# Kernel optimization log

Hardware: AMD Instinct MI355X
Metric: run time of the kernel (lower is better)

## Reference

```python
import jax, jax.numpy as jnp
import numpy as np

LOG2PI = float(np.log(2.0 * np.pi))
NUM_GROUPS = 32
WEIGHTS_THRESHOLD = 0.01
ACTIVATION_THRESHOLD = 1e-9


def _cdist(a, b):
    # a: (..., N, 3), b: (..., M, 3) -> (..., N, M) euclidean distances
    d2 = (jnp.sum(a * a, -1)[..., :, None]
          + jnp.sum(b * b, -1)[..., None, :]
          - 2.0 * jnp.einsum('...nd,...md->...nm', a, b))
    return jnp.sqrt(jnp.maximum(d2, 0.0))


def setup_inputs() -> dict:
    key = jax.random.key(0)
    ks = jax.random.split(key, 7)
    B, V, O, G = 16, 778, 8192, NUM_GROUPS
    verts = jax.random.normal(ks[0], (B, V, 3), jnp.float32)
    anchor_verts = jax.random.normal(ks[1], (B, G, 3), jnp.float32)
    obj_pts = jax.random.normal(ks[2], (B, O, 3), jnp.float32)
    raw = jax.random.normal(ks[3], (B, G, 12), jnp.float32)
    mean = raw[..., :3]
    M = raw[..., 3:].reshape(B, G, 3, 3)
    cov = jnp.einsum('bgij,bgkj->bgik', M, M) + 1e-2 * jnp.eye(3, dtype=jnp.float32)
    contact_gaussians = jnp.concatenate([mean, cov.reshape(B, G, 9)], axis=-1)
    obj_normals = jax.random.normal(ks[4], (B, O, 6), jnp.float32)
    init_verts = jax.random.normal(ks[5], (V, 3), jnp.float32)
    init_anchors = jax.random.normal(ks[6], (G, 3), jnp.float32)
    return dict(verts=verts, anchor_verts=anchor_verts, obj_pts=obj_pts,
                contact_gaussians=contact_gaussians, obj_normals=obj_normals,
                init_verts=init_verts, init_anchors=init_anchors, K=5)


def reference(verts, anchor_verts, obj_pts, contact_gaussians, obj_normals,
              init_verts, init_anchors, K):
    B, V, _ = verts.shape
    G = NUM_GROUPS
    # __init__: assign each vertex to its closest anchor (partition into 32 groups)
    gid = jnp.argmin(_cdist(init_verts, init_anchors), axis=-1)  # (V,)

    # KNN: K smallest distances vertex -> object points
    neigh = _cdist(verts, obj_pts)                 # (B, V, O)
    knn = -jax.lax.top_k(-neigh, K)[0]             # (B, V, K)

    # Per-group MVN log-prob for every vertex (G=32 small, V=778 small)
    mean = contact_gaussians[:, :, :3] + anchor_verts          # (B, G, 3)
    cov = contact_gaussians[:, :, 3:].reshape(B, G, 3, 3)
    L = jnp.linalg.cholesky(cov)                               # (B, G, 3, 3)
    diff = verts[:, None, :, :] - mean[:, :, None, :]          # (B, G, V, 3)
    y = jax.scipy.linalg.solve_triangular(L[:, :, None], diff[..., None], lower=True)[..., 0]
    maha = jnp.sum(y * y, -1)                                  # (B, G, V)
    half_logdet = jnp.sum(jnp.log(jnp.diagonal(L, axis1=-2, axis2=-1)), -1)  # (B, G)
    logp = -0.5 * (maha + 3.0 * LOG2PI) - half_logdet[:, :, None]
    w_all = jnp.exp(logp)                                      # (B, G, V)
    # pick each vertex's own group's weight
    idx = jnp.broadcast_to(gid[None, None, :], (B, 1, V))
    w = jnp.take_along_axis(w_all, idx, axis=1)[:, 0]          # (B, V)

    # per-group min/max normalization (masked, groups partition the vertices)
    grp_mask = gid[None, :] == jnp.arange(G)[:, None]          # (G, V)
    seg_min = jnp.min(jnp.where(grp_mask[None], w[:, None, :], jnp.inf), -1)   # (B, G)
    seg_max = jnp.max(jnp.where(grp_mask[None], w[:, None, :], -jnp.inf), -1)  # (B, G)
    mn = seg_min[:, gid]
    mx = seg_max[:, gid]
    wn = (w - mn) / (mx - mn)
    wn = jnp.where(wn > WEIGHTS_THRESHOLD, wn, 0.0)

    # group activation: torch.allclose(cg[:, i], 0) over whole batch -> zero weight
    active = jnp.any(jnp.abs(contact_gaussians) > ACTIVATION_THRESHOLD, axis=(0, 2))  # (G,)
    eff = jnp.where(active[gid][None, :], wn, 0.0)             # (B, V)
    distances = knn * eff[..., None]
    d_mean = jnp.mean(distances)

    # penetration regularizer using nearest object normal
    ovd = _cdist(verts, obj_normals[..., :3])                  # (B, V, O)
    nn_idx = jnp.argmin(ovd, -1)                               # (B, V)
    nn = jnp.take_along_axis(obj_normals, nn_idx[..., None], axis=1)  # (B, V, 6)
    roots = nn[..., :3] - 0.002 * nn[..., 3:]
    dp = jnp.einsum('bvi,bvi->bv', nn[..., 3:], verts - roots)
    pen = jnp.mean(jax.nn.relu(-dp))
    return (d_mean, pen)
```

## Files before the change

### kernel.cpp

```cpp
#include <hip/hip_runtime.h>
#include <math.h>

#define BB 16
#define VV 778
#define OO 8192
#define GG 32
#define KNN 5
#define THREE_LOG2PI 5.513631199228036f

#define MED3 __builtin_amdgcn_fmed3f

__device__ __forceinline__ void insert5_med3(float (&t)[KNN], float s) {
    t[4] = MED3(s, t[3], t[4]);
    t[3] = MED3(s, t[2], t[3]);
    t[2] = MED3(s, t[1], t[2]);
    t[1] = MED3(s, t[0], t[1]);
    t[0] = fminf(t[0], s);
}

__device__ __forceinline__ void merge5_med3(float (&m)[KNN], const float (&b)[KNN]) {
    m[4] = MED3(b[0], m[3], m[4]);
    m[3] = MED3(b[0], m[2], m[3]);
    m[2] = MED3(b[0], m[1], m[2]);
    m[1] = MED3(b[0], m[0], m[1]);
    m[0] = fminf(m[0], b[0]);
    m[4] = MED3(b[1], m[3], m[4]);
    m[3] = MED3(b[1], m[2], m[3]);
    m[2] = MED3(b[1], m[1], m[2]);
    m[1] = fminf(m[1], b[1]);
    m[4] = MED3(b[2], m[3], m[4]);
    m[3] = MED3(b[2], m[2], m[3]);
    m[2] = fminf(m[2], b[2]);
    m[4] = MED3(b[3], m[3], m[4]);
    m[3] = fminf(m[3], b[3]);
    m[4] = fminf(m[4], b[4]);
}

__device__ __forceinline__ unsigned int fkey(float s) {
    unsigned int u = __float_as_uint(s);
    unsigned int m = (u & 0x80000000u) ? 0xFFFFFFFFu : 0x80000000u;
    return u ^ m;
}

template <int LOGP1, int LOGP2>
__global__ __launch_bounds__(256) void scan_kernel(
    const float* __restrict__ verts,
    const float* __restrict__ anchor_verts,
    const float* __restrict__ obj_pts,
    const float* __restrict__ contact_gaussians,
    const float* __restrict__ obj_normals,
    const float* __restrict__ init_verts,
    const float* __restrict__ init_anchors,
    int* __restrict__ gid_ws,
    float* __restrict__ active_ws,
    float* __restrict__ segmn,
    float* __restrict__ segmx,
    float* __restrict__ w_ws,
    float* __restrict__ top5,
    unsigned long long* __restrict__ amin,
    float* __restrict__ out) {
    constexpr int P1 = 1 << LOGP1;
    constexpr int NPTS1 = OO >> LOGP1;
    constexpr int CH1 = (NPTS1 < 512) ? NPTS1 : 512;
    constexpr int P2 = 1 << LOGP2;
    constexpr int NPTS2 = OO >> LOGP2;
    constexpr int CH2 = (NPTS2 < 512) ? NPTS2 : 512;
    constexpr int CHMAX = (CH1 > CH2) ? CH1 : CH2;

    __shared__ float4 tile[CHMAX];
    __shared__ float anc[GG * 4];
    __shared__ float cholb[GG * 10];
    __shared__ unsigned short gidl[VV];
    __shared__ unsigned int smn[GG], smx[GG];

    int tid = threadIdx.x;
    int bid = blockIdx.x;

    if (bid < BB * P1) {
        int p = bid & (P1 - 1);
        int b = bid >> LOGP1;

        float X[4], Y[4], Z[4];
#pragma unroll
        for (int s = 0; s < 4; ++s) {
            int v = tid + s * 256;
            if (v >= VV) v = VV - 1;
            const float* vp = verts + ((size_t)b * VV + v) * 3;
            X[s] = -2.0f * vp[0];
            Y[s] = -2.0f * vp[1];
            Z[s] = -2.0f * vp[2];
        }

        float t[4][KNN];
#pragma unroll
        for (int s = 0; s < 4; ++s)
#pragma unroll
            for (int k = 0; k < KNN; ++k) t[s][k] = INFINITY;

        const float* pb = obj_pts + ((size_t)b * OO + p * NPTS1) * 3;
        for (int c0 = 0; c0 < NPTS1; c0 += CH1) {
            for (int j = tid; j < CH1; j += 256) {
                const float* q = pb + (size_t)(c0 + j) * 3;
                float a0 = q[0], a1 = q[1], a2 = q[2];
                tile[j] = make_float4(a0, a1, a2, a0 * a0 + a1 * a1 + a2 * a2);
            }
            __syncthreads();
#pragma unroll 4
            for (int i = 0; i < CH1; ++i) {
                float4 q = tile[i];
#pragma unroll
                for (int s = 0; s < 4; ++s) {
                    float sv = fmaf(X[s], q.x, fmaf(Y[s], q.y, fmaf(Z[s], q.z, q.w)));
                    insert5_med3(t[s], sv);
                }
            }
            __syncthreads();
        }
        {
            size_t base = ((size_t)(b * P1 + p) * KNN) * VV;
#pragma unroll
            for (int s = 0; s < 4; ++s) {
                int v = tid + s * 256;
                if (v < VV) {
#pragma unroll
                    for (int k = 0; k < KNN; ++k)
                        top5[base + (size_t)k * VV + v] = t[s][k];
                }
            }
        }
        return;
    }

    {
        int sub = bid - BB * P1;
        int p = sub & (P2 - 1);
        int b = sub >> LOGP2;

        bool wduty = (p == 0);
        bool aduty = (p == 1 && b == 0);
        if (wduty || aduty) {
            if (tid < GG) {
                float x = init_anchors[tid * 3 + 0];
                float y = init_anchors[tid * 3 + 1];
                float z = init_anchors[tid * 3 + 2];
                anc[tid * 4 + 0] = x; anc[tid * 4 + 1] = y;
                anc[tid * 4 + 2] = z; anc[tid * 4 + 3] = x * x + y * y + z * z;
                smn[tid] = 0x7F800000u;
                smx[tid] = 0u;
                if (wduty) {
                    const float* cg2 = contact_gaussians + ((size_t)b * GG + tid) * 12;
                    const float* av = anchor_verts + ((size_t)b * GG + tid) * 3;
                    float c00 = cg2[3];
                    float c10 = cg2[6], c11 = cg2[7];
                    float c20 = cg2[9], c21 = cg2[10], c22 = cg2[11];
                    float L00 = sqrtf(c00);
                    float L10 = c10 / L00;
                    float L20 = c20 / L00;
                    float L11 = sqrtf(c11 - L10 * L10);
                    float L21 = (c21 - L20 * L10) / L11;
                    float L22 = sqrtf(c22 - L20 * L20 - L21 * L21);
                    float* c = cholb + tid * 10;
                    c[0] = L00; c[1] = L10; c[2] = L11;
                    c[3] = L20; c[4] = L21; c[5] = L22;
                    c[6] = logf(L00) + logf(L11) + logf(L22);
                    c[7] = cg2[0] + av[0];
                    c[8] = cg2[1] + av[1];
                    c[9] = cg2[2] + av[2];
                }
            }
            __syncthreads();
            for (int v = tid; v < VV; v += 256) {
                float x = init_verts[v * 3 + 0];
                float y = init_verts[v * 3 + 1];
                float z = init_verts[v * 3 + 2];
                float vv = x * x + y * y + z * z;
                float best = INFINITY;
                int bg = 0;
                for (int g = 0; g < GG; ++g) {
                    float d2 = vv + anc[g * 4 + 3] -
                               2.0f * (x * anc[g * 4 + 0] + y * anc[g * 4 + 1] + z * anc[g * 4 + 2]);
                    d2 = fmaxf(d2, 0.0f);
                    if (d2 < best) { best = d2; bg = g; }
                }
                gidl[v] = (unsigned short)bg;
                if (aduty) gid_ws[v] = bg;
            }
            __syncthreads();
            if (wduty) {
                for (int v = tid; v < VV; v += 256) {
                    int g = gidl[v];
                    const float* c = cholb + g * 10;
                    const float* vp = verts + ((size_t)b * VV + v) * 3;
                    float d0 = vp[0] - c[7];
                    float d1 = vp[1] - c[8];
                    float d2 = vp[2] - c[9];
                    float y0 = d0 / c[0];
                    float y1 = (d1 - c[1] * y0) / c[2];
                    float y2 = (d2 - c[3] * y0 - c[4] * y1) / c[5];
                    float maha = y0 * y0 + y1 * y1 + y2 * y2;
                    float wv = expf(-0.5f * (maha + THREE_LOG2PI) - c[6]);
                    w_ws[(size_t)b * VV + v] = wv;
                    unsigned int u = __float_as_uint(wv);
                    atomicMin(&smn[g], u);
                    atomicMax(&smx[g], u);
                }
                __syncthreads();
                if (tid < GG) {
                    segmn[b * GG + tid] = __uint_as_float(smn[tid]);
                    segmx[b * GG + tid] = __uint_as_float(smx[tid]);
                }
            }
            if (aduty) {
                if (tid < GG) {
                    int any = 0;
                    for (int bb = 0; bb < BB && !any; ++bb) {
                        for (int c = 0; c < 12; ++c) {
                            if (fabsf(contact_gaussians[((size_t)bb * GG + tid) * 12 + c]) > 1e-9f) {
                                any = 1;
                                break;
                            }
                        }
                    }
                    active_ws[tid] = any ? 1.0f : 0.0f;
                }
                if (tid == 0) { out[0] = 0.0f; out[1] = 0.0f; }
            }
            __syncthreads();
        }

        float X[4], Y[4], Z[4];
#pragma unroll
        for (int s = 0; s < 4; ++s) {
            int v = tid + s * 256;
            if (v >= VV) v = VV - 1;
            const float* vp = verts + ((size_t)b * VV + v) * 3;
            X[s] = -2.0f * vp[0];
            Y[s] = -2.0f * vp[1];
            Z[s] = -2.0f * vp[2];
        }

        float bs[4];
        int bi[4];
#pragma unroll
        for (int s = 0; s < 4; ++s) { bs[s] = INFINITY; bi[s] = 0; }

        const float* nbp = obj_normals + ((size_t)b * OO + p * NPTS2) * 6;
        for (int c0 = 0; c0 < NPTS2; c0 += CH2) {
            for (int j = tid; j < CH2; j += 256) {
                const float* r = nbp + (size_t)(c0 + j) * 6;
                float b0 = r[0], b1 = r[1], b2 = r[2];
                tile[j] = make_float4(b0, b1, b2, b0 * b0 + b1 * b1 + b2 * b2);
            }
            __syncthreads();
#pragma unroll 4
            for (int i = 0; i < CH2; ++i) {
                float4 n = tile[i];
                int gi = c0 + i;
#pragma unroll
                for (int s = 0; s < 4; ++s) {
                    float u = fmaf(X[s], n.x, fmaf(Y[s], n.y, fmaf(Z[s], n.z, n.w)));
                    if (u < bs[s]) { bs[s] = u; bi[s] = gi; }
                }
            }
            __syncthreads();
        }
#pragma unroll
        for (int s = 0; s < 4; ++s) {
            int v = tid + s * 256;
            if (v < VV) {
                unsigned long long key =
                    ((unsigned long long)fkey(bs[s]) << 32) |
                    (unsigned int)(p * NPTS2 + bi[s]);
                atomicMin(&amin[(size_t)b * VV + v], key);
            }
        }
    }
}

template <int LOGP1>
__global__ __launch_bounds__(256) void finalize_kernel(
    const float* __restrict__ top5,
    const unsigned long long* __restrict__ amin,
    const float* __restrict__ obj_normals,
    const float* __restrict__ verts,
    const int* __restrict__ gid,
    const float* __restrict__ w,
    const float* __restrict__ segmn,
    const float* __restrict__ segmx,
    const float* __restrict__ active,
    float* __restrict__ out) {
    constexpr int P1 = 1 << LOGP1;
    constexpr int NM1 = (P1 + 3) / 4;
    constexpr int NCH = (VV + 63) / 64;

    __shared__ float mt[4][KNN][64];
    __shared__ float rd[256], rp[256];

    int tid = threadIdx.x;
    int pi = tid >> 6;
    int vi = tid & 63;
    int b = blockIdx.x / NCH;
    int chunk = blockIdx.x - b * NCH;
    int v = chunk * 64 + vi;
    bool valid = v < VV;

    float m[KNN];
#pragma unroll
    for (int k = 0; k < KNN; ++k) m[k] = INFINITY;
    if (valid) {
#pragma unroll
        for (int r = 0; r < NM1; ++r) {
            int p = pi * NM1 + r;
            if (p < P1) {
                size_t base = ((size_t)(b * P1 + p) * KNN) * VV + v;
                float t[KNN];
#pragma unroll
                for (int k = 0; k < KNN; ++k) t[k] = top5[base + (size_t)k * VV];
                merge5_med3(m, t);
            }
        }
    }

#pragma unroll
    for (int k = 0; k < KNN; ++k) mt[pi][k][vi] = m[k];
    __syncthreads();

    if (pi < 2) {
        float t[KNN];
#pragma unroll
        for (int k = 0; k < KNN; ++k) t[k] = mt[pi + 2][k][vi];
        merge5_med3(m, t);
#pragma unroll
        for (int k = 0; k < KNN; ++k) mt[pi][k][vi] = m[k];
    }
    __syncthreads();

    float cd = 0.0f, cp = 0.0f;
    if (pi == 0 && valid) {
        float t[KNN];
#pragma unroll
        for (int k = 0; k < KNN; ++k) t[k] = mt[1][k][vi];
        merge5_med3(m, t);

        const float* vp = verts + ((size_t)b * VV + v) * 3;
        float vx = vp[0], vy = vp[1], vz = vp[2];
        float vv = vx * vx + vy * vy + vz * vz;

        int g = gid[v];
        float wv = w[(size_t)b * VV + v];
        float mn = segmn[b * GG + g];
        float mx = segmx[b * GG + g];
        float wn = (wv - mn) / (mx - mn);
        float eff = (active[g] != 0.0f && wn > 0.01f) ? wn : 0.0f;
        float sk = 0.0f;
#pragma unroll
        for (int k = 0; k < KNN; ++k) sk += sqrtf(fmaxf(vv + m[k], 0.0f));
        cd = eff * sk;

        int bi = (int)(unsigned int)(amin[(size_t)b * VV + v] & 0xFFFFFFFFull);
        const float* row = obj_normals + ((size_t)b * OO + bi) * 6;
        float n0 = row[3], n1 = row[4], n2 = row[5];
        float r0 = row[0] - 0.002f * n0;
        float r1 = row[1] - 0.002f * n1;
        float r2 = row[2] - 0.002f * n2;
        float dp = n0 * (vx - r0) + n1 * (vy - r1) + n2 * (vz - r2);
        cp = fmaxf(-dp, 0.0f);
    }

    rd[tid] = cd;
    rp[tid] = cp;
    __syncthreads();
    for (int s = 128; s > 0; s >>= 1) {
        if (tid < s) {
            rd[tid] += rd[tid + s];
            rp[tid] += rp[tid + s];
        }
        __syncthreads();
    }
    if (tid == 0) {
        atomicAdd(&out[0], rd[0] * (1.0f / ((float)BB * VV * KNN)));
        atomicAdd(&out[1], rp[0] * (1.0f / ((float)BB * VV)));
    }
}

template <int LOGP>
static void launch_all(const float* verts, const float* anchor_verts,
                       const float* obj_pts, const float* contact_gaussians,
                       const float* obj_normals, const float* init_verts,
                       const float* init_anchors, int* gid_ws, float* active_ws,
                       float* segmn, float* segmx, float* w_ws, float* top5,
                       unsigned long long* amin, float* out, hipStream_t stream) {
    constexpr int P = 1 << LOGP;
    constexpr int NCH = (VV + 63) / 64;
    dim3 block(256);
    hipLaunchKernelGGL((scan_kernel<LOGP, LOGP>), dim3(BB * 2 * P), block,
                       0, stream, verts, anchor_verts, obj_pts, contact_gaussians,
                       obj_normals, init_verts, init_anchors, gid_ws, active_ws,
                       segmn, segmx, w_ws, top5, amin, out);
    hipLaunchKernelGGL((finalize_kernel<LOGP>), dim3(BB * NCH), block, 0, stream,
                       top5, amin, obj_normals, verts, gid_ws, w_ws, segmn,
                       segmx, active_ws, out);
}

extern "C" void kernel_launch(void* const* d_in, const int* in_sizes, int n_in,
                              void* d_out, int out_size, void* d_ws, size_t ws_size,
                              hipStream_t stream) {
    const float* verts = (const float*)d_in[0];
    const float* anchor_verts = (const float*)d_in[1];
    const float* obj_pts = (const float*)d_in[2];
    const float* contact_gaussians = (const float*)d_in[3];
    const float* obj_normals = (const float*)d_in[4];
    const float* init_verts = (const float*)d_in[5];
    const float* init_anchors = (const float*)d_in[6];
    float* out = (float*)d_out;

    char* ws = (char*)d_ws;
    int* gid_ws = (int*)(ws + 0);
    float* active_ws = (float*)(ws + 4096);
    float* segmn = (float*)(ws + 4224);
    float* segmx = (float*)(ws + 6272);
    float* w_ws = (float*)(ws + 8320);
    unsigned long long* amin = (unsigned long long*)(ws + 58112);
    const size_t base = 157696;

    int logP = 5;
    while (logP > 0 &&
           base + (size_t)BB * (1 << logP) * KNN * VV * 4 > ws_size)
        --logP;

    float* top5 = (float*)(ws + base);

    hipMemsetAsync(amin, 0xFF, (size_t)BB * VV * sizeof(unsigned long long),
                   stream);

#define LAUNCH(L)                                                              \
    launch_all<L>(verts, anchor_verts, obj_pts, contact_gaussians,             \
                  obj_normals, init_verts, init_anchors, gid_ws, active_ws,    \
                  segmn, segmx, w_ws, top5, amin, out, stream)
    switch (logP) {
        case 5: LAUNCH(5); break;
        case 4: LAUNCH(4); break;
        case 3: LAUNCH(3); break;
        case 2: LAUNCH(2); break;
        case 1: LAUNCH(1); break;
        default: LAUNCH(0); break;
    }
#undef LAUNCH
}
```

Before: 140.4 us.

## Fuse finalize into scan kernel via last-block-done atomic counters

```diff
diff --git a/kernel.cpp b/kernel.cpp
--- a/kernel.cpp
+++ b/kernel.cpp
@@ -42,8 +42,8 @@
     return u ^ m;
 }
 
-template <int LOGP1, int LOGP2>
-__global__ __launch_bounds__(256) void scan_kernel(
+template <int LOGP>
+__global__ __launch_bounds__(256) void fused_kernel(
     const float* __restrict__ verts,
     const float* __restrict__ anchor_verts,
     const float* __restrict__ obj_pts,
@@ -52,33 +52,35 @@
     const float* __restrict__ init_verts,
     const float* __restrict__ init_anchors,
     int* __restrict__ gid_ws,
-    float* __restrict__ active_ws,
     float* __restrict__ segmn,
     float* __restrict__ segmx,
     float* __restrict__ w_ws,
     float* __restrict__ top5,
     unsigned long long* __restrict__ amin,
+    int* __restrict__ cnt,
+    int* __restrict__ cnt_all,
+    float* __restrict__ Sgrp,
+    float* __restrict__ Pb,
     float* __restrict__ out) {
-    constexpr int P1 = 1 << LOGP1;
-    constexpr int NPTS1 = OO >> LOGP1;
-    constexpr int CH1 = (NPTS1 < 512) ? NPTS1 : 512;
-    constexpr int P2 = 1 << LOGP2;
-    constexpr int NPTS2 = OO >> LOGP2;
-    constexpr int CH2 = (NPTS2 < 512) ? NPTS2 : 512;
-    constexpr int CHMAX = (CH1 > CH2) ? CH1 : CH2;
-
-    __shared__ float4 tile[CHMAX];
+    constexpr int P = 1 << LOGP;
+    constexpr int NPTS = OO >> LOGP;
+    constexpr int CH = (NPTS < 512) ? NPTS : 512;
+
+    __shared__ float4 tile[CH];
     __shared__ float anc[GG * 4];
     __shared__ float cholb[GG * 10];
     __shared__ unsigned short gidl[VV];
     __shared__ unsigned int smn[GG], smx[GG];
+    __shared__ int winflag, allflag;
 
     int tid = threadIdx.x;
     int bid = blockIdx.x;
-
-    if (bid < BB * P1) {
-        int p = bid & (P1 - 1);
-        int b = bid >> LOGP1;
+    int myb;
+
+    if (bid < BB * P) {
+        int p = bid & (P - 1);
+        int b = bid >> LOGP;
+        myb = b;
 
         float X[4], Y[4], Z[4];
 #pragma unroll
@@ -97,16 +99,16 @@
 #pragma unroll
             for (int k = 0; k < KNN; ++k) t[s][k] = INFINITY;
 
-        const float* pb = obj_pts + ((size_t)b * OO + p * NPTS1) * 3;
-        for (int c0 = 0; c0 < NPTS1; c0 += CH1) {
-            for (int j = tid; j < CH1; j += 256) {
+        const float* pb = obj_pts + ((size_t)b * OO + p * NPTS) * 3;
+        for (int c0 = 0; c0 < NPTS; c0 += CH) {
+            for (int j = tid; j < CH; j += 256) {
                 const float* q = pb + (size_t)(c0 + j) * 3;
                 float a0 = q[0], a1 = q[1], a2 = q[2];
                 tile[j] = make_float4(a0, a1, a2, a0 * a0 + a1 * a1 + a2 * a2);
             }
             __syncthreads();
 #pragma unroll 4
-            for (int i = 0; i < CH1; ++i) {
+            for (int i = 0; i < CH; ++i) {
                 float4 q = tile[i];
 #pragma unroll
                 for (int s = 0; s < 4; ++s) {
@@ -117,7 +119,7 @@
             __syncthreads();
         }
         {
-            size_t base = ((size_t)(b * P1 + p) * KNN) * VV;
+            size_t base = ((size_t)(b * P + p) * KNN) * VV;
 #pragma unroll
             for (int s = 0; s < 4; ++s) {
                 int v = tid + s * 256;
@@ -128,17 +130,14 @@
                 }
             }
         }
-        return;
-    }
-
-    {
-        int sub = bid - BB * P1;
-        int p = sub & (P2 - 1);
-        int b = sub >> LOGP2;
+    } else {
+        int sub = bid - BB * P;
+        int p = sub & (P - 1);
+        int b = sub >> LOGP;
+        myb = b;
 
         bool wduty = (p == 0);
-        bool aduty = (p == 1 && b == 0);
-        if (wduty || aduty) {
+        if (wduty) {
             if (tid < GG) {
                 float x = init_anchors[tid * 3 + 0];
                 float y = init_anchors[tid * 3 + 1];
@@ -147,26 +146,24 @@
                 anc[tid * 4 + 2] = z; anc[tid * 4 + 3] = x * x + y * y + z * z;
                 smn[tid] = 0x7F800000u;
                 smx[tid] = 0u;
-                if (wduty) {
-                    const float* cg2 = contact_gaussians + ((size_t)b * GG + tid) * 12;
-                    const float* av = anchor_verts + ((size_t)b * GG + tid) * 3;
-                    float c00 = cg2[3];
-                    float c10 = cg2[6], c11 = cg2[7];
-                    float c20 = cg2[9], c21 = cg2[10], c22 = cg2[11];
-                    float L00 = sqrtf(c00);
-                    float L10 = c10 / L00;
-                    float L20 = c20 / L00;
-                    float L11 = sqrtf(c11 - L10 * L10);
-                    float L21 = (c21 - L20 * L10) / L11;
-                    float L22 = sqrtf(c22 - L20 * L20 - L21 * L21);
-                    float* c = cholb + tid * 10;
-                    c[0] = L00; c[1] = L10; c[2] = L11;
-                    c[3] = L20; c[4] = L21; c[5] = L22;
-                    c[6] = logf(L00) + logf(L11) + logf(L22);
-                    c[7] = cg2[0] + av[0];
-                    c[8] = cg2[1] + av[1];
-                    c[9] = cg2[2] + av[2];
-                }
+                const float* cg2 = contact_gaussians + ((size_t)b * GG + tid) * 12;
+                const float* av = anchor_verts + ((size_t)b * GG + tid) * 3;
+                float c00 = cg2[3];
+                float c10 = cg2[6], c11 = cg2[7];
+                float c20 = cg2[9], c21 = cg2[10], c22 = cg2[11];
+                float L00 = sqrtf(c00);
+                float L10 = c10 / L00;
+                float L20 = c20 / L00;
+                float L11 = sqrtf(c11 - L10 * L10);
+                float L21 = (c21 - L20 * L10) / L11;
+                float L22 = sqrtf(c22 - L20 * L20 - L21 * L21);
+                float* c = cholb + tid * 10;
+                c[0] = L00; c[1] = L10; c[2] = L11;
+                c[3] = L20; c[4] = L21; c[5] = L22;
+                c[6] = logf(L00) + logf(L11) + logf(L22);
+                c[7] = cg2[0] + av[0];
+                c[8] = cg2[1] + av[1];
+                c[9] = cg2[2] + av[2];
             }
             __syncthreads();
             for (int v = tid; v < VV; v += 256) {
@@ -183,47 +180,30 @@
                     if (d2 < best) { best = d2; bg = g; }
                 }
                 gidl[v] = (unsigned short)bg;
-                if (aduty) gid_ws[v] = bg;
-            }
-            __syncthreads();
-            if (wduty) {
-                for (int v = tid; v < VV; v += 256) {
-                    int g = gidl[v];
-                    const float* c = cholb + g * 10;
-                    const float* vp = verts + ((size_t)b * VV + v) * 3;
-                    float d0 = vp[0] - c[7];
-                    float d1 = vp[1] - c[8];
-                    float d2 = vp[2] - c[9];
-                    float y0 = d0 / c[0];
-                    float y1 = (d1 - c[1] * y0) / c[2];
-                    float y2 = (d2 - c[3] * y0 - c[4] * y1) / c[5];
-                    float maha = y0 * y0 + y1 * y1 + y2 * y2;
-                    float wv = expf(-0.5f * (maha + THREE_LOG2PI) - c[6]);
-                    w_ws[(size_t)b * VV + v] = wv;
-                    unsigned int u = __float_as_uint(wv);
-                    atomicMin(&smn[g], u);
-                    atomicMax(&smx[g], u);
-                }
-                __syncthreads();
-                if (tid < GG) {
-                    segmn[b * GG + tid] = __uint_as_float(smn[tid]);
-                    segmx[b * GG + tid] = __uint_as_float(smx[tid]);
-                }
-            }
-            if (aduty) {
-                if (tid < GG) {
-                    int any = 0;
-                    for (int bb = 0; bb < BB && !any; ++bb) {
-                        for (int c = 0; c < 12; ++c) {
-                            if (fabsf(contact_gaussians[((size_t)bb * GG + tid) * 12 + c]) > 1e-9f) {
-                                any = 1;
-                                break;
-                            }
-                        }
-                    }
-                    active_ws[tid] = any ? 1.0f : 0.0f;
-                }
-                if (tid == 0) { out[0] = 0.0f; out[1] = 0.0f; }
+                gid_ws[v] = bg;
+            }
+            __syncthreads();
+            for (int v = tid; v < VV; v += 256) {
+                int g = gidl[v];
+                const float* c = cholb + g * 10;
+                const float* vp = verts + ((size_t)b * VV + v) * 3;
+                float d0 = vp[0] - c[7];
+                float d1 = vp[1] - c[8];
+                float d2 = vp[2] - c[9];
+                float y0 = d0 / c[0];
+                float y1 = (d1 - c[1] * y0) / c[2];
+                float y2 = (d2 - c[3] * y0 - c[4] * y1) / c[5];
+                float maha = y0 * y0 + y1 * y1 + y2 * y2;
+                float wv = expf(-0.5f * (maha + THREE_LOG2PI) - c[6]);
+                w_ws[(size_t)b * VV + v] = wv;
+                unsigned int u = __float_as_uint(wv);
+                atomicMin(&smn[g], u);
+                atomicMax(&smx[g], u);
+            }
+            __syncthreads();
+            if (tid < GG) {
+                segmn[b * GG + tid] = __uint_as_float(smn[tid]);
+                segmx[b * GG + tid] = __uint_as_float(smx[tid]);
             }
             __syncthreads();
         }
@@ -244,16 +224,16 @@
 #pragma unroll
         for (int s = 0; s < 4; ++s) { bs[s] = INFINITY; bi[s] = 0; }
 
-        const float* nbp = obj_normals + ((size_t)b * OO + p * NPTS2) * 6;
-        for (int c0 = 0; c0 < NPTS2; c0 += CH2) {
-            for (int j = tid; j < CH2; j += 256) {
+        const float* nbp = obj_normals + ((size_t)b * OO + p * NPTS) * 6;
+        for (int c0 = 0; c0 < NPTS; c0 += CH) {
+            for (int j = tid; j < CH; j += 256) {
                 const float* r = nbp + (size_t)(c0 + j) * 6;
                 float b0 = r[0], b1 = r[1], b2 = r[2];
                 tile[j] = make_float4(b0, b1, b2, b0 * b0 + b1 * b1 + b2 * b2);
             }
             __syncthreads();
 #pragma unroll 4
-            for (int i = 0; i < CH2; ++i) {
+            for (int i = 0; i < CH; ++i) {
                 float4 n = tile[i];
                 int gi = c0 + i;
 #pragma unroll
@@ -270,92 +250,55 @@
             if (v < VV) {
                 unsigned long long key =
                     ((unsigned long long)fkey(bs[s]) << 32) |
-                    (unsigned int)(p * NPTS2 + bi[s]);
+                    (unsigned int)(p * NPTS + bi[s]);
                 atomicMin(&amin[(size_t)b * VV + v], key);
             }
         }
     }
-}
-
-template <int LOGP1>
-__global__ __launch_bounds__(256) void finalize_kernel(
-    const float* __restrict__ top5,
-    const unsigned long long* __restrict__ amin,
-    const float* __restrict__ obj_normals,
-    const float* __restrict__ verts,
-    const int* __restrict__ gid,
-    const float* __restrict__ w,
-    const float* __restrict__ segmn,
-    const float* __restrict__ segmx,
-    const float* __restrict__ active,
-    float* __restrict__ out) {
-    constexpr int P1 = 1 << LOGP1;
-    constexpr int NM1 = (P1 + 3) / 4;
-    constexpr int NCH = (VV + 63) / 64;
-
-    __shared__ float mt[4][KNN][64];
-    __shared__ float rd[256], rp[256];
-
-    int tid = threadIdx.x;
-    int pi = tid >> 6;
-    int vi = tid & 63;
-    int b = blockIdx.x / NCH;
-    int chunk = blockIdx.x - b * NCH;
-    int v = chunk * 64 + vi;
-    bool valid = v < VV;
-
-    float m[KNN];
-#pragma unroll
-    for (int k = 0; k < KNN; ++k) m[k] = INFINITY;
-    if (valid) {
-#pragma unroll
-        for (int r = 0; r < NM1; ++r) {
-            int p = pi * NM1 + r;
-            if (p < P1) {
-                size_t base = ((size_t)(b * P1 + p) * KNN) * VV + v;
-                float t[KNN];
-#pragma unroll
-                for (int k = 0; k < KNN; ++k) t[k] = top5[base + (size_t)k * VV];
-                merge5_med3(m, t);
-            }
-        }
-    }
-
-#pragma unroll
-    for (int k = 0; k < KNN; ++k) mt[pi][k][vi] = m[k];
-    __syncthreads();
-
-    if (pi < 2) {
-        float t[KNN];
-#pragma unroll
-        for (int k = 0; k < KNN; ++k) t[k] = mt[pi + 2][k][vi];
-        merge5_med3(m, t);
-#pragma unroll
-        for (int k = 0; k < KNN; ++k) mt[pi][k][vi] = m[k];
-    }
-    __syncthreads();
-
-    float cd = 0.0f, cp = 0.0f;
-    if (pi == 0 && valid) {
-        float t[KNN];
-#pragma unroll
-        for (int k = 0; k < KNN; ++k) t[k] = mt[1][k][vi];
-        merge5_med3(m, t);
+
+    __syncthreads();
+    __threadfence();
+    if (tid == 0) {
+        int prev = atomicAdd(&cnt[myb], 1);
+        winflag = (prev == 2 * P - 1);
+    }
+    __syncthreads();
+    if (!winflag) return;
+
+    __threadfence();
+    int b = myb;
+    float* sgrp = anc;
+    float* redp = (float*)tile;
+    if (tid < GG) sgrp[tid] = 0.0f;
+    float penacc = 0.0f;
+    __syncthreads();
+
+    for (int v = tid; v < VV; v += 256) {
+        float m[KNN];
+#pragma unroll
+        for (int k = 0; k < KNN; ++k) m[k] = INFINITY;
+        for (int p = 0; p < P; ++p) {
+            size_t base = ((size_t)(b * P + p) * KNN) * VV + v;
+            float t[KNN];
+#pragma unroll
+            for (int k = 0; k < KNN; ++k) t[k] = top5[base + (size_t)k * VV];
+            merge5_med3(m, t);
+        }
 
         const float* vp = verts + ((size_t)b * VV + v) * 3;
         float vx = vp[0], vy = vp[1], vz = vp[2];
         float vv = vx * vx + vy * vy + vz * vz;
 
-        int g = gid[v];
-        float wv = w[(size_t)b * VV + v];
+        int g = gid_ws[v];
+        float wv = w_ws[(size_t)b * VV + v];
         float mn = segmn[b * GG + g];
         float mx = segmx[b * GG + g];
         float wn = (wv - mn) / (mx - mn);
-        float eff = (active[g] != 0.0f && wn > 0.01f) ? wn : 0.0f;
+        float eff = (wn > 0.01f) ? wn : 0.0f;
         float sk = 0.0f;
 #pragma unroll
         for (int k = 0; k < KNN; ++k) sk += sqrtf(fmaxf(vv + m[k], 0.0f));
-        cd = eff * sk;
+        atomicAdd(&sgrp[g], eff * sk);
 
         int bi = (int)(unsigned int)(amin[(size_t)b * VV + v] & 0xFFFFFFFFull);
         const float* row = obj_normals + ((size_t)b * OO + bi) * 6;
@@ -364,42 +307,64 @@
         float r1 = row[1] - 0.002f * n1;
         float r2 = row[2] - 0.002f * n2;
         float dp = n0 * (vx - r0) + n1 * (vy - r1) + n2 * (vz - r2);
-        cp = fmaxf(-dp, 0.0f);
-    }
-
-    rd[tid] = cd;
-    rp[tid] = cp;
+        penacc += fmaxf(-dp, 0.0f);
+    }
+
+    redp[tid] = penacc;
     __syncthreads();
     for (int s = 128; s > 0; s >>= 1) {
-        if (tid < s) {
-            rd[tid] += rd[tid + s];
-            rp[tid] += rp[tid + s];
-        }
+        if (tid < s) redp[tid] += redp[tid + s];
         __syncthreads();
     }
+    if (tid == 0) Pb[b] = redp[0];
+    if (tid < GG) Sgrp[b * GG + tid] = sgrp[tid];
+
+    __syncthreads();
+    __threadfence();
     if (tid == 0) {
-        atomicAdd(&out[0], rd[0] * (1.0f / ((float)BB * VV * KNN)));
-        atomicAdd(&out[1], rp[0] * (1.0f / ((float)BB * VV)));
-    }
-}
-
-template <int LOGP>
-static void launch_all(const float* verts, const float* anchor_verts,
-                       const float* obj_pts, const float* contact_gaussians,
-                       const float* obj_normals, const float* init_verts,
-                       const float* init_anchors, int* gid_ws, float* active_ws,
-                       float* segmn, float* segmx, float* w_ws, float* top5,
-                       unsigned long long* amin, float* out, hipStream_t stream) {
-    constexpr int P = 1 << LOGP;
-    constexpr int NCH = (VV + 63) / 64;
-    dim3 block(256);
-    hipLaunchKernelGGL((scan_kernel<LOGP, LOGP>), dim3(BB * 2 * P), block,
-                       0, stream, verts, anchor_verts, obj_pts, contact_gaussians,
-                       obj_normals, init_verts, init_anchors, gid_ws, active_ws,
-                       segmn, segmx, w_ws, top5, amin, out);
-    hipLaunchKernelGGL((finalize_kernel<LOGP>), dim3(BB * NCH), block, 0, stream,
-                       top5, amin, obj_normals, verts, gid_ws, w_ws, segmn,
-                       segmx, active_ws, out);
+        int prev = atomicAdd(cnt_all, 1);
+        allflag = (prev == BB - 1);
+    }
+    __syncthreads();
+    if (!allflag) return;
+
+    __threadfence();
+    float* actf = cholb;
+    if (tid < GG) {
+        int any = 0;
+        for (int bb = 0; bb < BB && !any; ++bb) {
+            for (int c = 0; c < 12; ++c) {
+                if (fabsf(contact_gaussians[((size_t)bb * GG + tid) * 12 + c]) > 1e-9f) {
+                    any = 1;
+                    break;
+                }
+            }
+        }
+        actf[tid] = any ? 1.0f : 0.0f;
+    }
+    __syncthreads();
+
+    float sd = 0.0f;
+    for (int i = tid; i < BB * GG; i += 256) sd += actf[i & (GG - 1)] * Sgrp[i];
+    float sp = (tid < BB) ? Pb[tid] : 0.0f;
+    redp[tid] = sd;
+    __syncthreads();
+    for (int s = 128; s > 0; s >>= 1) {
+        if (tid < s) redp[tid] += redp[tid + s];
+        __syncthreads();
+    }
+    float total_d = redp[0];
+    __syncthreads();
+    redp[tid] = sp;
+    __syncthreads();
+    for (int s = 128; s > 0; s >>= 1) {
+        if (tid < s) redp[tid] += redp[tid + s];
+        __syncthreads();
+    }
+    if (tid == 0) {
+        out[0] = total_d * (1.0f / ((float)BB * VV * KNN));
+        out[1] = redp[0] * (1.0f / ((float)BB * VV));
+    }
 }
 
 extern "C" void kernel_launch(void* const* d_in, const int* in_sizes, int n_in,
@@ -416,12 +381,15 @@
 
     char* ws = (char*)d_ws;
     int* gid_ws = (int*)(ws + 0);
-    float* active_ws = (float*)(ws + 4096);
-    float* segmn = (float*)(ws + 4224);
-    float* segmx = (float*)(ws + 6272);
-    float* w_ws = (float*)(ws + 8320);
-    unsigned long long* amin = (unsigned long long*)(ws + 58112);
-    const size_t base = 157696;
+    float* segmn = (float*)(ws + 4096);
+    float* segmx = (float*)(ws + 6144);
+    float* w_ws = (float*)(ws + 8192);
+    unsigned long long* amin = (unsigned long long*)(ws + 58368);
+    int* cnt = (int*)(ws + 157952);
+    int* cnt_all = (int*)(ws + 158016);
+    float* Sgrp = (float*)(ws + 158080);
+    float* Pb = (float*)(ws + 160128);
+    const size_t base = 160256;
 
     int logP = 5;
     while (logP > 0 &&
@@ -432,11 +400,14 @@
 
     hipMemsetAsync(amin, 0xFF, (size_t)BB * VV * sizeof(unsigned long long),
                    stream);
+    hipMemsetAsync(cnt, 0, 17 * sizeof(int), stream);
 
 #define LAUNCH(L)                                                              \
-    launch_all<L>(verts, anchor_verts, obj_pts, contact_gaussians,             \
-                  obj_normals, init_verts, init_anchors, gid_ws, active_ws,    \
-                  segmn, segmx, w_ws, top5, amin, out, stream)
+    hipLaunchKernelGGL((fused_kernel<L>), dim3(BB * 2 * (1 << L)), dim3(256),  \
+                       0, stream, verts, anchor_verts, obj_pts,                \
+                       contact_gaussians, obj_normals, init_verts,             \
+                       init_anchors, gid_ws, segmn, segmx, w_ws, top5, amin,   \
+                       cnt, cnt_all, Sgrp, Pb, out)
     switch (logP) {
         case 5: LAUNCH(5); break;
         case 4: LAUNCH(4); break;
```

Measured after the change: 223.1 us. 58.9% more time.
